# Kernel tuning notes

Measured on AMD Instinct MI355X. Metric: run time of the kernel, lower is better.

Reference implementation:

```python
import jax, jax.numpy as jnp
import numpy as np

N, E, G = 50000, 800000, 128          # nodes, edges, graphs
L, T, F = 4, 4, 20                    # conv layers, towers, per-tower width
D = T * F                             # 80 = hidden dim
EDGE_DIM = 16
AVG_DEG_LOG = float(np.log(17.0))     # avg_deg['log'] for avg in-degree ~16
EPS_STD = 1e-5
EPS_BN = 1e-5


def setup_inputs() -> dict:
    ks = iter(jax.random.split(jax.random.key(0), 32))
    rn = lambda *s: jax.random.normal(next(ks), s, jnp.float32) * 0.1
    return dict(
        x=jax.random.randint(next(ks), (N, 9), 0, 16),
        edge_index=jax.random.randint(next(ks), (2, E), 0, N),
        batch=jnp.sort(jax.random.randint(next(ks), (N,), 0, G)),
        edge_attr=rn(E, EDGE_DIM),
        atom_emb=rn(9, 16, D),
        edge_w=rn(L, EDGE_DIM, F), edge_b=jnp.zeros((L, F), jnp.float32),
        pre_w1=rn(L, T, 3 * F, F), pre_b1=jnp.zeros((L, T, F), jnp.float32),
        pre_w2=rn(L, T, F, F), pre_b2=jnp.zeros((L, T, F), jnp.float32),
        post_w1=rn(L, T, 13 * F, F), post_b1=jnp.zeros((L, T, F), jnp.float32),
        post_w2=rn(L, T, F, F), post_b2=jnp.zeros((L, T, F), jnp.float32),
        lin_w=rn(L, D, D), lin_b=jnp.zeros((L, D), jnp.float32),
        bn_g=jnp.ones((L, D), jnp.float32), bn_b=jnp.zeros((L, D), jnp.float32),
        mlp_w1=rn(D, 40), mlp_b1=jnp.zeros(40, jnp.float32),
        mlp_w2=rn(40, 20), mlp_b2=jnp.zeros(20, jnp.float32),
        mlp_w3=rn(20, 1), mlp_b3=jnp.zeros(1, jnp.float32),
    )


def _net(x, edge_index, batch, edge_attr, atom_emb, edge_w, edge_b, pre_w1,
         pre_b1, pre_w2, pre_b2, post_w1, post_b1, post_w2, post_b2, lin_w,
         lin_b, bn_g, bn_b, mlp_w1, mlp_b1, mlp_w2, mlp_b2, mlp_w3, mlp_b3):
    src, dst = edge_index[0], edge_index[1]
    # AtomEncoder: sum of 9 categorical embeddings -> [N, D]
    h = atom_emb[jnp.arange(9)[None, :], x].sum(1)
    deg_raw = jax.ops.segment_sum(jnp.ones((E,), jnp.float32), dst, N)
    deg = jnp.clip(deg_raw, 1.0)
    has_edge = (deg_raw > 0)[:, None, None]
    d3 = deg[:, None, None]
    logd = jnp.log(deg + 1.0)[:, None, None]
    for l in range(L):  # 4 PNAConv + BN + ReLU + residual (dropout off / eval)
        xt = h.reshape(N, T, F)
        ea = edge_attr @ edge_w[l] + edge_b[l]                      # [E, F]
        # message: concat(x_i, x_j, edge) -> per-tower pre MLP
        m = jnp.concatenate([xt[dst], xt[src],
                             jnp.broadcast_to(ea[:, None, :], (E, T, F))], -1)
        m = jax.nn.relu(jnp.einsum('eti,tio->eto', m, pre_w1[l]) + pre_b1[l])
        m = jnp.einsum('eti,tio->eto', m, pre_w2[l]) + pre_b2[l]    # [E,T,F]
        # multi-aggregator scatter-reduce
        mean = jax.ops.segment_sum(m, dst, N) / d3
        msq = jax.ops.segment_sum(m * m, dst, N) / d3
        std = jnp.sqrt(jax.nn.relu(msq - mean * mean) + EPS_STD)
        mn = jnp.where(has_edge, jax.ops.segment_min(m, dst, N), 0.0)
        mx = jnp.where(has_edge, jax.ops.segment_max(m, dst, N), 0.0)
        agg = jnp.concatenate([mean, mn, mx, std], -1)              # [N,T,4F]
        # degree scalers: identity, amplification, attenuation
        out = jnp.concatenate([agg, agg * (logd / AVG_DEG_LOG),
                               agg * (AVG_DEG_LOG / logd)], -1)     # [N,T,12F]
        out = jnp.concatenate([xt, out], -1)                        # [N,T,13F]
        out = jax.nn.relu(jnp.einsum('nti,tio->nto', out, post_w1[l]) + post_b1[l])
        out = jnp.einsum('nti,tio->nto', out, post_w2[l]) + post_b2[l]
        out = out.reshape(N, D) @ lin_w[l] + lin_b[l]
        # BatchNorm over nodes (batch statistics)
        mu = out.mean(0)
        var = jnp.mean((out - mu) ** 2, axis=0)
        out = (out - mu) * (bn_g[l] / jnp.sqrt(var + EPS_BN)) + bn_b[l]
        h = jax.nn.relu(out) + h
    # global mean pool over graphs + readout MLP
    cnt = jnp.clip(jax.ops.segment_sum(jnp.ones((N,), jnp.float32), batch, G), 1.0)
    g = jax.ops.segment_sum(h, batch, G) / cnt[:, None]
    g = jax.nn.relu(g @ mlp_w1 + mlp_b1)
    g = jax.nn.relu(g @ mlp_w2 + mlp_b2)
    return g @ mlp_w3 + mlp_b3                                      # [G, 1]


def reference(x, edge_index, batch, edge_attr, atom_emb, edge_w, edge_b, pre_w1,
              pre_b1, pre_w2, pre_b2, post_w1, post_b1, post_w2, post_b2, lin_w,
              lin_b, bn_g, bn_b, mlp_w1, mlp_b1, mlp_w2, mlp_b2, mlp_w3, mlp_b3):
    return _net(x, edge_index, batch, edge_attr, atom_emb, edge_w, edge_b, pre_w1,
                pre_b1, pre_w2, pre_b2, post_w1, post_b1, post_w2, post_b2,
                lin_w, lin_b, bn_g, bn_b, mlp_w1, mlp_b1, mlp_w2, mlp_b2,
                mlp_w3, mlp_b3)
```

## Files before the change

### kernel.cpp

```cpp
#include <hip/hip_runtime.h>
#include <hip/hip_bf16.h>

#define NN 50000
#define EE 800000
#define GG 128
#define LL 4
#define TT 4
#define FF 20
#define DD 80
#define SCAN_B ((NN + 1023) / 1024)
static constexpr float AVG_LOG = 2.8332133440562162f;

typedef __fp16 half2v __attribute__((ext_vector_type(2)));

__device__ __forceinline__ float bf2f(unsigned short u) {
  return __uint_as_float((unsigned)u << 16);
}
__device__ __forceinline__ unsigned short f2bf(float f) {
  __hip_bfloat16 b = __float2bfloat16(f);
  return *(unsigned short*)&b;
}
__device__ __forceinline__ half2v pkrtz(float a, float b) {
#if __has_builtin(__builtin_amdgcn_cvt_pkrtz)
  return __builtin_amdgcn_cvt_pkrtz(a, b);
#else
  half2v h; h.x = (__fp16)a; h.y = (__fp16)b; return h;
#endif
}
__device__ __forceinline__ float fdot2(half2v a, half2v b, float c) {
#if __has_builtin(__builtin_amdgcn_fdot2)
  return __builtin_amdgcn_fdot2(a, b, c, false);
#else
  return fmaf((float)a.x, (float)b.x, fmaf((float)a.y, (float)b.y, c));
#endif
}
__device__ __forceinline__ half2v u2h2(unsigned int u) {
  return __builtin_bit_cast(half2v, u);
}
__device__ __forceinline__ unsigned int h22u(half2v h) {
  return __builtin_bit_cast(unsigned int, h);
}
__device__ __forceinline__ unsigned int packh2_rne(float a, float b) {
  half2v h; h.x = (__fp16)a; h.y = (__fp16)b;
  return h22u(h);
}
__device__ __forceinline__ unsigned int pack_bf16(float a, float b) {
  return (unsigned int)f2bf(a) | ((unsigned int)f2bf(b) << 16);
}

__global__ __launch_bounds__(256) void k_h(const int* __restrict__ x,
                                           const float* __restrict__ atom_emb,
                                           float* __restrict__ h) {
  int idx = blockIdx.x * 256 + threadIdx.x;
  if (idx >= NN * DD) return;
  int n = idx / DD, d = idx - n * DD;
  const int* xr = x + n * 9;
  float acc = 0.f;
#pragma unroll
  for (int i = 0; i < 9; ++i) {
    int v = xr[i];
    acc += atom_emb[(i * 16 + v) * DD + d];
  }
  h[idx] = acc;
}

__global__ __launch_bounds__(256) void k_deg(const int* __restrict__ ei, int* __restrict__ cnt) {
  int e = blockIdx.x * 256 + threadIdx.x;
  if (e >= EE) return;
  atomicAdd(&cnt[ei[EE + e]], 1);
}

__global__ __launch_bounds__(1024) void k_scan_sum(const int* __restrict__ cnt, int* __restrict__ bsum) {
  __shared__ int red[1024];
  int tid = threadIdx.x;
  int i = blockIdx.x * 1024 + tid;
  red[tid] = (i < NN) ? cnt[i] : 0;
  __syncthreads();
  for (int off = 512; off > 0; off >>= 1) {
    if (tid < off) red[tid] += red[tid + off];
    __syncthreads();
  }
  if (tid == 0) bsum[blockIdx.x] = red[0];
}

__global__ void k_scan_top(const int* __restrict__ bsum, int* __restrict__ boff,
                           int* __restrict__ row_ptr) {
  if (threadIdx.x == 0 && blockIdx.x == 0) {
    int acc = 0;
    for (int b = 0; b < SCAN_B; ++b) { boff[b] = acc; acc += bsum[b]; }
    row_ptr[NN] = acc;
  }
}

__global__ __launch_bounds__(1024) void k_scan_apply(const int* __restrict__ cnt,
                                                     const int* __restrict__ boff,
                                                     int* __restrict__ row_ptr,
                                                     int* __restrict__ cursor) {
  __shared__ int sm[1024];
  int tid = threadIdx.x;
  int i = blockIdx.x * 1024 + tid;
  int v = (i < NN) ? cnt[i] : 0;
  sm[tid] = v;
  __syncthreads();
  for (int off = 1; off < 1024; off <<= 1) {
    int t = (tid >= off) ? sm[tid - off] : 0;
    __syncthreads();
    sm[tid] += t;
    __syncthreads();
  }
  int excl = boff[blockIdx.x] + sm[tid] - v;
  if (i < NN) { row_ptr[i] = excl; cursor[i] = excl; }
}

__global__ __launch_bounds__(256) void k_csrfill(const int* __restrict__ ei,
                                                 int* __restrict__ cursor,
                                                 int2* __restrict__ csr2,
                                                 int* __restrict__ csr_dst) {
  int e = blockIdx.x * 256 + threadIdx.x;
  if (e >= EE) return;
  int dst = ei[EE + e];
  int slot = atomicAdd(&cursor[dst], 1);
  csr2[slot] = make_int2(ei[e], e);
  csr_dst[slot] = dst;
}

__global__ __launch_bounds__(256) void k_eagather(const int2* __restrict__ csr2,
                                                  const float* __restrict__ edge_attr,
                                                  unsigned int* __restrict__ ea16) {
  int sl = blockIdx.x * 256 + threadIdx.x;
  if (sl >= EE) return;
  int e = csr2[sl].y;
  const float4* ap = (const float4*)(edge_attr + (size_t)e * 16);
  uint4 o0, o1;
  float4 v0 = ap[0], v1 = ap[1], v2 = ap[2], v3 = ap[3];
  o0.x = packh2_rne(v0.x, v0.y); o0.y = packh2_rne(v0.z, v0.w);
  o0.z = packh2_rne(v1.x, v1.y); o0.w = packh2_rne(v1.z, v1.w);
  o1.x = packh2_rne(v2.x, v2.y); o1.y = packh2_rne(v2.z, v2.w);
  o1.z = packh2_rne(v3.x, v3.y); o1.w = packh2_rne(v3.z, v3.w);
  uint4* op = (uint4*)(ea16 + (size_t)sl * 8);
  op[0] = o0; op[1] = o1;
}

__global__ __launch_bounds__(256) void k_nodeparams(const int* __restrict__ cnt,
                                                    float* __restrict__ inv_deg,
                                                    float* __restrict__ s1a,
                                                    float* __restrict__ s2a) {
  int n = blockIdx.x * 256 + threadIdx.x;
  if (n >= NN) return;
  int c = cnt[n];
  float deg = (c > 0) ? (float)c : 1.0f;
  inv_deg[n] = 1.0f / deg;
  float logd = logf(deg + 1.0f);
  s1a[n] = logd / AVG_LOG;
  s2a[n] = AVG_LOG / logd;
}

__global__ __launch_bounds__(64) void k_wcomb(const float* __restrict__ edge_w,
                                              const float* __restrict__ edge_b,
                                              const float* __restrict__ pre_w1,
                                              const float* __restrict__ pre_b1,
                                              const float* __restrict__ pre_w2,
                                              unsigned int* __restrict__ wcpk,
                                              unsigned int* __restrict__ w2pk,
                                              float* __restrict__ biasc, int l) {
  int t = blockIdx.x;
  int wt = l * TT + t;
  const float* W1 = pre_w1 + (size_t)wt * 1200;
  const float* W2 = pre_w2 + (size_t)wt * 400;
  const float* ew = edge_w + (size_t)l * 16 * FF;
  const float* eb = edge_b + (size_t)l * FF;
  int j = threadIdx.x;
  if (j >= FF) return;
  float col[16];
  for (int i = 0; i < 16; ++i) {
    float acc = 0.f;
#pragma unroll
    for (int f = 0; f < FF; ++f) acc = fmaf(ew[i * FF + f], W1[(40 + f) * FF + j], acc);
    col[i] = acc;
  }
#pragma unroll
  for (int i2 = 0; i2 < 8; ++i2)
    wcpk[((size_t)t * FF + j) * 8 + i2] = packh2_rne(col[2 * i2], col[2 * i2 + 1]);
#pragma unroll
  for (int i2 = 0; i2 < 10; ++i2)
    w2pk[((size_t)t * FF + j) * 10 + i2] = packh2_rne(W2[(2 * i2) * FF + j], W2[(2 * i2 + 1) * FF + j]);
  float b = pre_b1[wt * FF + j];
#pragma unroll
  for (int f = 0; f < FF; ++f) b = fmaf(eb[f], W1[(40 + f) * FF + j], b);
  biasc[t * FF + j] = b;
}

__global__ __launch_bounds__(64) void k_postpk(const float* __restrict__ post_w1,
                                               const float* __restrict__ post_w2,
                                               unsigned int* __restrict__ q1pk,
                                               unsigned int* __restrict__ q2pk, int l) {
  int t = blockIdx.x;
  int wt = l * TT + t;
  const float* Q1 = post_w1 + (size_t)wt * 5200;
  const float* Q2 = post_w2 + (size_t)wt * 400;
  int j = threadIdx.x;
  if (j >= FF) return;
  for (int i2 = 0; i2 < 120; ++i2) {
    int blk = i2 / 40, k = i2 - blk * 40;
    int r0 = 20 + 80 * blk + 2 * k;
    q1pk[((size_t)t * 120 + i2) * FF + j] = packh2_rne(Q1[r0 * FF + j], Q1[(r0 + 1) * FF + j]);
  }
#pragma unroll
  for (int i2 = 0; i2 < 10; ++i2)
    q2pk[((size_t)t * 10 + i2) * FF + j] = packh2_rne(Q2[(2 * i2) * FF + j], Q2[(2 * i2 + 1) * FF + j]);
}

__global__ __launch_bounds__(256) void k_prenode(
    const float* __restrict__ h, const float* __restrict__ pre_w1,
    const float* __restrict__ biasc,
    unsigned short* __restrict__ predD, unsigned short* __restrict__ predS, int l) {
  int tid = threadIdx.x;
  int t = tid >> 6, lane = tid & 63;
  int n = blockIdx.x * 64 + lane;
  if (n >= NN) return;
  int wt_u = __builtin_amdgcn_readfirstlane(l * TT + t);
  const float* W1 = pre_w1 + (size_t)wt_u * 1200;
  const float* bc = biasc + t * FF;
  float xt[FF];
  {
    const float4* pp = (const float4*)(h + (size_t)n * DD + t * FF);
#pragma unroll
    for (int i = 0; i < 5; ++i) { float4 v = pp[i]; xt[i*4]=v.x; xt[i*4+1]=v.y; xt[i*4+2]=v.z; xt[i*4+3]=v.w; }
  }
  float d[FF], s[FF];
#pragma unroll
  for (int j = 0; j < FF; ++j) { d[j] = bc[j]; s[j] = 0.f; }
#pragma unroll
  for (int i = 0; i < FF; ++i) {
    float a = xt[i];
#pragma unroll
    for (int j = 0; j < FF; ++j) {
      d[j] = fmaf(a, W1[i * FF + j], d[j]);
      s[j] = fmaf(a, W1[(FF + i) * FF + j], s[j]);
    }
  }
  ushort4* pd = (ushort4*)(predD + (size_t)n * DD + t * FF);
  ushort4* ps = (ushort4*)(predS + (size_t)n * DD + t * FF);
#pragma unroll
  for (int i = 0; i < 5; ++i) {
    pd[i] = make_ushort4(f2bf(d[i*4]), f2bf(d[i*4+1]), f2bf(d[i*4+2]), f2bf(d[i*4+3]));
    ps[i] = make_ushort4(f2bf(s[i*4]), f2bf(s[i*4+1]), f2bf(s[i*4+2]), f2bf(s[i*4+3]));
  }
}

__global__ __launch_bounds__(256, 4) void k_pre(
    const unsigned short* __restrict__ predD, const unsigned short* __restrict__ predS,
    const unsigned int* __restrict__ ea16,
    const int2* __restrict__ csr2, const int* __restrict__ csr_dst,
    const int* __restrict__ row_ptr,
    const unsigned int* __restrict__ wcpk,
    const unsigned int* __restrict__ w2pk,
    const float* __restrict__ pre_b2,
    unsigned int* __restrict__ m, int l, int n0, int n1, int capSlots) {
  int tid = threadIdx.x;
  int t = tid >> 6;
  int lane = tid & 63;
  int wt_u = __builtin_amdgcn_readfirstlane(l * TT + t);
  int t_u  = __builtin_amdgcn_readfirstlane(t);
  const unsigned int* Wcp = wcpk + (size_t)t_u * FF * 8;
  const unsigned int* W2p = w2pk + (size_t)t_u * FF * 10;
  const float* b2 = pre_b2 + (size_t)wt_u * FF;

  int sl = blockIdx.x * 64 + lane;
  int base = row_ptr[n0], end = row_ptr[n1];
  if (sl >= capSlots || base + sl >= end) return;
  int p = base + sl;
  int src = csr2[p].x;
  int dst = csr_dst[p];

  float m1[FF];
  {
    const ushort4* pp = (const ushort4*)(predD + (size_t)dst * DD + t * FF);
    const ushort4* qq = (const ushort4*)(predS + (size_t)src * DD + t * FF);
#pragma unroll
    for (int i = 0; i < 5; ++i) {
      ushort4 u = pp[i];
      ushort4 v = qq[i];
      m1[i*4+0] = bf2f(u.x) + bf2f(v.x);
      m1[i*4+1] = bf2f(u.y) + bf2f(v.y);
      m1[i*4+2] = bf2f(u.z) + bf2f(v.z);
      m1[i*4+3] = bf2f(u.w) + bf2f(v.w);
    }
  }
  half2v eap[8];
  {
    const uint4* ep = (const uint4*)(ea16 + (size_t)p * 8);
    uint4 e0 = ep[0], e1 = ep[1];
    eap[0] = u2h2(e0.x); eap[1] = u2h2(e0.y); eap[2] = u2h2(e0.z); eap[3] = u2h2(e0.w);
    eap[4] = u2h2(e1.x); eap[5] = u2h2(e1.y); eap[6] = u2h2(e1.z); eap[7] = u2h2(e1.w);
  }
#pragma unroll
  for (int j = 0; j < FF; ++j) {
    float c = m1[j];
#pragma unroll
    for (int i2 = 0; i2 < 8; ++i2) c = fdot2(eap[i2], u2h2(Wcp[j * 8 + i2]), c);
    m1[j] = c;
  }
  half2v mp[10];
#pragma unroll
  for (int pr = 0; pr < 10; ++pr)
    mp[pr] = pkrtz(fmaxf(m1[2*pr], 0.f), fmaxf(m1[2*pr+1], 0.f));
  float m2[FF];
#pragma unroll
  for (int j = 0; j < FF; ++j) {
    float c = b2[j];
#pragma unroll
    for (int i2 = 0; i2 < 10; ++i2) c = fdot2(mp[i2], u2h2(W2p[j * 10 + i2]), c);
    m2[j] = c;
  }
  unsigned int* mrow = m + (size_t)t * 10 * capSlots + sl;
#pragma unroll
  for (int pr = 0; pr < 10; ++pr)
    mrow[(size_t)pr * capSlots] = h22u(pkrtz(m2[2*pr], m2[2*pr+1]));
}

__global__ __launch_bounds__(320) void k_agg(
    const unsigned int* __restrict__ m,
    const int* __restrict__ row_ptr,
    const float* __restrict__ inv_deg,
    unsigned short* __restrict__ aggbuf, int n0, int n1, int capSlots) {
  int tid = threadIdx.x;
  int t = blockIdx.x & 3, tile = blockIdx.x >> 2;
  int ni = tid / 10, pr = tid - ni * 10;
  int n = n0 + tile * 32 + ni;
  if (n >= n1) return;
  int base = row_ptr[n0];
  int beg = row_ptr[n], end = row_ptr[n + 1];
  float inv = inv_deg[n];
  int s0 = beg - base, s1c = end - base;
  if (s0 < 0) s0 = 0;
  if (s1c > capSlots) s1c = capSlots;
  float sum0 = 0.f, sum1 = 0.f, sq0 = 0.f, sq1 = 0.f;
  float mn0 = 3.4e38f, mn1 = 3.4e38f, mx0 = -3.4e38f, mx1 = -3.4e38f;
  const unsigned int* mrow = m + (size_t)(t * 10 + pr) * capSlots;
  int p = s0;
  for (; p < s1c && (p & 3); ++p) {
    half2v h = u2h2(mrow[p]);
    float v0 = (float)h.x, v1 = (float)h.y;
    sum0 += v0; sq0 = fmaf(v0, v0, sq0); mn0 = fminf(mn0, v0); mx0 = fmaxf(mx0, v0);
    sum1 += v1; sq1 = fmaf(v1, v1, sq1); mn1 = fminf(mn1, v1); mx1 = fmaxf(mx1, v1);
  }
  for (; p + 4 <= s1c; p += 4) {
    uint4 q = *(const uint4*)(mrow + p);
#pragma unroll
    for (int k = 0; k < 4; ++k) {
      unsigned int u = (k == 0) ? q.x : (k == 1) ? q.y : (k == 2) ? q.z : q.w;
      half2v h = u2h2(u);
      float v0 = (float)h.x, v1 = (float)h.y;
      sum0 += v0; sq0 = fmaf(v0, v0, sq0); mn0 = fminf(mn0, v0); mx0 = fmaxf(mx0, v0);
      sum1 += v1; sq1 = fmaf(v1, v1, sq1); mn1 = fminf(mn1, v1); mx1 = fmaxf(mx1, v1);
    }
  }
  for (; p < s1c; ++p) {
    half2v h = u2h2(mrow[p]);
    float v0 = (float)h.x, v1 = (float)h.y;
    sum0 += v0; sq0 = fmaf(v0, v0, sq0); mn0 = fminf(mn0, v0); mx0 = fmaxf(mx0, v0);
    sum1 += v1; sq1 = fmaf(v1, v1, sq1); mn1 = fminf(mn1, v1); mx1 = fmaxf(mx1, v1);
  }
  float mu0 = sum0 * inv, mu1 = sum1 * inv;
  float sd0 = sqrtf(fmaxf(sq0 * inv - mu0 * mu0, 0.f) + 1e-5f);
  float sd1 = sqrtf(fmaxf(sq1 * inv - mu1 * mu1, 0.f) + 1e-5f);
  if (end <= beg) { mn0 = 0.f; mn1 = 0.f; mx0 = 0.f; mx1 = 0.f; }
  unsigned short* ab = aggbuf + ((size_t)(n - n0) * 4 + t) * 80;
  ((unsigned int*)(ab))[pr]      = pack_bf16(mu0, mu1);
  ((unsigned int*)(ab + 20))[pr] = pack_bf16(mn0, mn1);
  ((unsigned int*)(ab + 40))[pr] = pack_bf16(mx0, mx1);
  ((unsigned int*)(ab + 60))[pr] = pack_bf16(sd0, sd1);
}

__global__ __launch_bounds__(256) void k_post2(
    const float* __restrict__ h, const unsigned short* __restrict__ aggbuf,
    const float* __restrict__ s1a, const float* __restrict__ s2a,
    const float* __restrict__ post_w1, const float* __restrict__ post_b1,
    const unsigned int* __restrict__ q1pk, const unsigned int* __restrict__ q2pk,
    const float* __restrict__ post_b2,
    float* __restrict__ out2, int l, int n0, int n1, int tiles) {
  int t = blockIdx.x / tiles;
  int tile = blockIdx.x - t * tiles;
  int wt_u = l * TT + t;
  const float* Q1 = post_w1 + (size_t)wt_u * 5200;
  const float* B1 = post_b1 + (size_t)wt_u * FF;
  const float* B2 = post_b2 + (size_t)wt_u * FF;
  const unsigned int* q1 = q1pk + (size_t)t * 120 * FF;
  const unsigned int* q2 = q2pk + (size_t)t * 10 * FF;
  int n = n0 + tile * 256 + threadIdx.x;
  if (n >= n1) return;
  float c1 = s1a[n], c2 = s2a[n];
  half2v c1p = pkrtz(c1, c1), c2p = pkrtz(c2, c2);
  float xt[FF];
  {
    const float4* pp = (const float4*)(h + (size_t)n * DD + t * FF);
#pragma unroll
    for (int i = 0; i < 5; ++i) { float4 v = pp[i]; xt[i*4]=v.x; xt[i*4+1]=v.y; xt[i*4+2]=v.z; xt[i*4+3]=v.w; }
  }
  half2v a0p[40];
  {
    const uint4* ap = (const uint4*)(aggbuf + ((size_t)(n - n0) * 4 + t) * 80);
#pragma unroll
    for (int q = 0; q < 10; ++q) {
      uint4 v = ap[q];
      unsigned int w[4] = {v.x, v.y, v.z, v.w};
#pragma unroll
      for (int k = 0; k < 4; ++k) {
        unsigned int u = w[k];
        float lo = __uint_as_float(u << 16);
        float hi = __uint_as_float(u & 0xffff0000u);
        a0p[q * 4 + k] = pkrtz(lo, hi);
      }
    }
  }
  float o1[FF];
#pragma unroll
  for (int j = 0; j < FF; ++j) o1[j] = B1[j];
#pragma unroll
  for (int i = 0; i < FF; ++i) {
    float a = xt[i];
#pragma unroll
    for (int j = 0; j < FF; ++j) o1[j] = fmaf(a, Q1[i * FF + j], o1[j]);
  }
#pragma unroll 2
  for (int k = 0; k < 40; ++k) {
    half2v act = a0p[k];
    const unsigned int* wr = q1 + k * FF;
#pragma unroll
    for (int j = 0; j < FF; ++j) o1[j] = fdot2(act, u2h2(wr[j]), o1[j]);
  }
#pragma unroll 2
  for (int k = 0; k < 40; ++k) {
    half2v act = a0p[k] * c1p;
    const unsigned int* wr = q1 + (40 + k) * FF;
#pragma unroll
    for (int j = 0; j < FF; ++j) o1[j] = fdot2(act, u2h2(wr[j]), o1[j]);
  }
#pragma unroll 2
  for (int k = 0; k < 40; ++k) {
    half2v act = a0p[k] * c2p;
    const unsigned int* wr = q1 + (80 + k) * FF;
#pragma unroll
    for (int j = 0; j < FF; ++j) o1[j] = fdot2(act, u2h2(wr[j]), o1[j]);
  }
  half2v o1p[10];
#pragma unroll
  for (int i2 = 0; i2 < 10; ++i2)
    o1p[i2] = pkrtz(fmaxf(o1[2*i2], 0.f), fmaxf(o1[2*i2+1], 0.f));
  float o2[FF];
#pragma unroll
  for (int j = 0; j < FF; ++j) o2[j] = B2[j];
#pragma unroll 2
  for (int i2 = 0; i2 < 10; ++i2) {
    half2v act = o1p[i2];
    const unsigned int* wr = q2 + i2 * FF;
#pragma unroll
    for (int j = 0; j < FF; ++j) o2[j] = fdot2(act, u2h2(wr[j]), o2[j]);
  }
  float4* op = (float4*)(out2 + (size_t)n * DD + t * FF);
#pragma unroll
  for (int i = 0; i < 5; ++i) op[i] = make_float4(o2[i*4], o2[i*4+1], o2[i*4+2], o2[i*4+3]);
}

__global__ __launch_bounds__(320) void k_lin(const float* __restrict__ out2,
                                             const float* __restrict__ lin_w,
                                             const float* __restrict__ lin_b,
                                             float* __restrict__ outl,
                                             float* __restrict__ colsum, int l) {
  __shared__ float Wl[DD * DD];
  __shared__ float rowbuf[4 * DD];
  __shared__ float red[320];
  int tid = threadIdx.x;
  for (int i = tid; i < DD * DD; i += 320) Wl[i] = lin_w[(size_t)l * DD * DD + i];
  __syncthreads();
  int nl = tid / DD, d = tid - nl * DD;
  float bias = lin_b[l * DD + d];
  float bsum = 0.f, bsq = 0.f;
  for (int base = blockIdx.x * 4; base < NN; base += gridDim.x * 4) {
    int gi = base * DD + tid;
    rowbuf[tid] = (gi < NN * DD) ? out2[gi] : 0.f;
    __syncthreads();
    int n = base + nl;
    if (n < NN) {
      float acc = bias;
#pragma unroll
      for (int i = 0; i < DD; ++i) acc = fmaf(rowbuf[nl * DD + i], Wl[i * DD + d], acc);
      outl[(size_t)n * DD + d] = acc;
      bsum += acc; bsq += acc * acc;
    }
    __syncthreads();
  }
  red[tid] = bsum;
  __syncthreads();
  if (tid < DD) {
    float s = red[tid] + red[tid + DD] + red[tid + 2 * DD] + red[tid + 3 * DD];
    atomicAdd(&colsum[d], s);
  }
  __syncthreads();
  red[tid] = bsq;
  __syncthreads();
  if (tid < DD) {
    float s = red[tid] + red[tid + DD] + red[tid + 2 * DD] + red[tid + 3 * DD];
    atomicAdd(&colsum[DD + d], s);
  }
}

__global__ __launch_bounds__(128) void k_bnfinal(const float* __restrict__ colsum,
                                                 const float* __restrict__ bn_g,
                                                 const float* __restrict__ bn_b,
                                                 float* __restrict__ bnsc, int l) {
  int d = threadIdx.x;
  if (d >= DD) return;
  float mu = colsum[d] * (1.0f / NN);
  float var = colsum[DD + d] * (1.0f / NN) - mu * mu;
  float sc = bn_g[l * DD + d] * rsqrtf(var + 1e-5f);
  bnsc[d] = sc;
  bnsc[DD + d] = bn_b[l * DD + d] - mu * sc;
}

__global__ __launch_bounds__(256) void k_bnapply(const float* __restrict__ outl,
                                                 const float* __restrict__ bnsc,
                                                 float* __restrict__ h) {
  int idx = blockIdx.x * 256 + threadIdx.x;
  if (idx >= NN * DD) return;
  int d = idx % DD;
  float v = fmaf(outl[idx], bnsc[d], bnsc[DD + d]);
  h[idx] += fmaxf(v, 0.f);
}

__global__ __launch_bounds__(256) void k_gcnt(const int* __restrict__ batch, int* __restrict__ gcnt) {
  __shared__ int hcnt[GG];
  int tid = threadIdx.x;
  if (tid < GG) hcnt[tid] = 0;
  __syncthreads();
  int n = blockIdx.x * 256 + tid;
  if (n < NN) atomicAdd(&hcnt[batch[n]], 1);
  __syncthreads();
  if (tid < GG && hcnt[tid] > 0) atomicAdd(&gcnt[tid], hcnt[tid]);
}

__global__ void k_gstart(const int* __restrict__ gcnt, int* __restrict__ gstart) {
  if (threadIdx.x == 0 && blockIdx.x == 0) {
    int acc = 0;
    for (int g = 0; g < GG; ++g) { gstart[g] = acc; acc += gcnt[g]; }
  }
}

__global__ __launch_bounds__(320) void k_gmean(const float* __restrict__ h,
                                               const int* __restrict__ gstart,
                                               const int* __restrict__ gcnt,
                                               float* __restrict__ gbuf) {
  __shared__ float red[320];
  int g = blockIdx.x, tid = threadIdx.x;
  int nl = tid / DD, d = tid - nl * DD;
  int start = gstart[g], c = gcnt[g];
  float acc = 0.f;
  for (int r = start + nl; r < start + c; r += 4) acc += h[(size_t)r * DD + d];
  red[tid] = acc;
  __syncthreads();
  if (tid < DD) {
    float s = red[tid] + red[tid + DD] + red[tid + 2 * DD] + red[tid + 3 * DD];
    float cf = (c > 0) ? (float)c : 1.0f;
    gbuf[g * DD + tid] = s / cf;
  }
}

__global__ __launch_bounds__(64) void k_mlp(const float* __restrict__ gbuf,
                                            const float* __restrict__ w1, const float* __restrict__ b1,
                                            const float* __restrict__ w2, const float* __restrict__ b2,
                                            const float* __restrict__ w3, const float* __restrict__ b3,
                                            float* __restrict__ out) {
  __shared__ float row[DD];
  __shared__ float t1[40];
  __shared__ float t2[20];
  int g = blockIdx.x, tid = threadIdx.x;
  for (int i = tid; i < DD; i += 64) row[i] = gbuf[g * DD + i];
  __syncthreads();
  if (tid < 40) {
    float acc = b1[tid];
#pragma unroll
    for (int i = 0; i < DD; ++i) acc = fmaf(row[i], w1[i * 40 + tid], acc);
    t1[tid] = fmaxf(acc, 0.f);
  }
  __syncthreads();
  if (tid < 20) {
    float acc = b2[tid];
#pragma unroll
    for (int i = 0; i < 40; ++i) acc = fmaf(t1[i], w2[i * 20 + tid], acc);
    t2[tid] = fmaxf(acc, 0.f);
  }
  __syncthreads();
  if (tid == 0) {
    float acc = b3[0];
#pragma unroll
    for (int i = 0; i < 20; ++i) acc = fmaf(t2[i], w3[i], acc);
    out[g] = acc;
  }
}

extern "C" void kernel_launch(void* const* d_in, const int* in_sizes, int n_in,
                              void* d_out, int out_size, void* d_ws, size_t ws_size,
                              hipStream_t stream) {
  const int*   x         = (const int*)d_in[0];
  const int*   ei        = (const int*)d_in[1];
  const int*   batch     = (const int*)d_in[2];
  const float* edge_attr = (const float*)d_in[3];
  const float* atom_emb  = (const float*)d_in[4];
  const float* edge_w    = (const float*)d_in[5];
  const float* edge_b    = (const float*)d_in[6];
  const float* pre_w1    = (const float*)d_in[7];
  const float* pre_b1    = (const float*)d_in[8];
  const float* pre_w2    = (const float*)d_in[9];
  const float* pre_b2    = (const float*)d_in[10];
  const float* post_w1   = (const float*)d_in[11];
  const float* post_b1   = (const float*)d_in[12];
  const float* post_w2   = (const float*)d_in[13];
  const float* post_b2   = (const float*)d_in[14];
  const float* lin_w     = (const float*)d_in[15];
  const float* lin_b     = (const float*)d_in[16];
  const float* bn_g      = (const float*)d_in[17];
  const float* bn_b      = (const float*)d_in[18];
  const float* mlp_w1    = (const float*)d_in[19];
  const float* mlp_b1    = (const float*)d_in[20];
  const float* mlp_w2    = (const float*)d_in[21];
  const float* mlp_b2    = (const float*)d_in[22];
  const float* mlp_w3    = (const float*)d_in[23];
  const float* mlp_b3    = (const float*)d_in[24];
  float* out = (float*)d_out;

  char* ws = (char*)d_ws;
  size_t off = 0;
  auto alloc = [&](size_t bytes) -> void* {
    void* p = ws + off;
    off += (bytes + 15) & ~(size_t)15;
    return p;
  };
  float* h       = (float*)alloc((size_t)NN * DD * 4);
  float* out2    = (float*)alloc((size_t)NN * DD * 4);
  unsigned short* predD = (unsigned short*)alloc((size_t)NN * DD * 2);
  unsigned short* predS = (unsigned short*)alloc((size_t)NN * DD * 2);
  int2*  csr2    = (int2*)alloc((size_t)EE * 8);
  int*   csr_dst = (int*)alloc((size_t)EE * 4);
  unsigned int* ea16 = (unsigned int*)alloc((size_t)EE * 8 * 4);
  int*   row_ptr = (int*)alloc((size_t)(NN + 1) * 4);
  int*   cnt     = (int*)alloc((size_t)NN * 4);
  int*   cursor  = (int*)alloc((size_t)NN * 4);
  float* inv_deg = (float*)alloc((size_t)NN * 4);
  float* s1a     = (float*)alloc((size_t)NN * 4);
  float* s2a     = (float*)alloc((size_t)NN * 4);
  float* colsum  = (float*)alloc(2 * DD * 4);
  float* bnsc    = (float*)alloc(2 * DD * 4);
  float* gbuf    = (float*)alloc((size_t)GG * DD * 4);
  unsigned int* wcpk  = (unsigned int*)alloc((size_t)TT * FF * 8 * 4);
  unsigned int* w2pk  = (unsigned int*)alloc((size_t)TT * FF * 10 * 4);
  unsigned int* q1pk  = (unsigned int*)alloc((size_t)TT * 120 * FF * 4);
  unsigned int* q2pk  = (unsigned int*)alloc((size_t)TT * 10 * FF * 4);
  float* biasc   = (float*)alloc((size_t)TT * FF * 4);
  int*   bsum    = (int*)alloc((size_t)SCAN_B * 4);
  int*   boff    = (int*)alloc((size_t)SCAN_B * 4);
  int*   gcnt    = (int*)alloc((size_t)GG * 4);
  int*   gstart  = (int*)alloc((size_t)(GG + 1) * 4);
  (void)in_sizes; (void)n_in; (void)out_size;

  size_t rest = (ws_size > off) ? (ws_size - off) : 0;
  static const int cands[] = {1, 2, 4, 5, 8, 10, 20, 25, 40, 50};
  int c = -1, capSlots = 0, nodesPer = 0;
  size_t aggBytes = 0;
  for (int ci = 0; ci < 10; ++ci) {
    int cc = cands[ci];
    int np = (NN + cc - 1) / cc;
    size_t ab = ((size_t)np * 4 * 80 * 2 + 63) & ~(size_t)63;
    int slots = EE / cc + 25000; if (slots > EE) slots = EE;
    slots = (slots + 63) & ~63;
    size_t mb = (size_t)slots * DD * 2;
    if (ab + mb <= rest && ab + mb >= (size_t)NN * DD * 4) {
      c = cc; capSlots = slots; nodesPer = np; aggBytes = ab;
      break;
    }
  }
  if (c < 0) {
    c = 50; nodesPer = (NN + c - 1) / c;
    aggBytes = ((size_t)nodesPer * 4 * 80 * 2 + 63) & ~(size_t)63;
    size_t mb = (rest > aggBytes) ? rest - aggBytes : 0;
    capSlots = (int)(mb / (DD * 2)) & ~63;
  }
  unsigned short* aggbuf = (unsigned short*)(ws + off);
  unsigned int* mbuf = (unsigned int*)(ws + off + aggBytes);
  float* outl = (float*)(ws + off);

  hipMemsetAsync(cnt, 0, (size_t)NN * 4, stream);
  k_h<<<(NN * DD + 255) / 256, 256, 0, stream>>>(x, atom_emb, h);
  k_deg<<<(EE + 255) / 256, 256, 0, stream>>>(ei, cnt);
  k_scan_sum<<<SCAN_B, 1024, 0, stream>>>(cnt, bsum);
  k_scan_top<<<1, 64, 0, stream>>>(bsum, boff, row_ptr);
  k_scan_apply<<<SCAN_B, 1024, 0, stream>>>(cnt, boff, row_ptr, cursor);
  k_csrfill<<<(EE + 255) / 256, 256, 0, stream>>>(ei, cursor, csr2, csr_dst);
  k_eagather<<<(EE + 255) / 256, 256, 0, stream>>>(csr2, edge_attr, ea16);
  k_nodeparams<<<(NN + 255) / 256, 256, 0, stream>>>(cnt, inv_deg, s1a, s2a);

  for (int l = 0; l < LL; ++l) {
    k_wcomb<<<TT, 64, 0, stream>>>(edge_w, edge_b, pre_w1, pre_b1, pre_w2, wcpk, w2pk, biasc, l);
    k_postpk<<<TT, 64, 0, stream>>>(post_w1, post_w2, q1pk, q2pk, l);
    k_prenode<<<(NN + 63) / 64, 256, 0, stream>>>(h, pre_w1, biasc, predD, predS, l);
    for (int ck = 0; ck < c; ++ck) {
      int n0 = ck * nodesPer;
      int n1 = n0 + nodesPer; if (n1 > NN) n1 = NN;
      if (n0 >= n1) continue;
      int preBlocks = (capSlots + 63) / 64;
      k_pre<<<preBlocks, 256, 0, stream>>>(predD, predS, ea16, csr2, csr_dst, row_ptr,
          wcpk, w2pk, pre_b2, mbuf, l, n0, n1, capSlots);
      int aggBlocks = ((n1 - n0 + 31) / 32) * 4;
      k_agg<<<aggBlocks, 320, 0, stream>>>(mbuf, row_ptr, inv_deg, aggbuf, n0, n1, capSlots);
      int tiles = (n1 - n0 + 255) / 256;
      k_post2<<<tiles * TT, 256, 0, stream>>>(h, aggbuf, s1a, s2a,
          post_w1, post_b1, q1pk, q2pk, post_b2, out2, l, n0, n1, tiles);
    }
    hipMemsetAsync(colsum, 0, 2 * DD * 4, stream);
    k_lin<<<512, 320, 0, stream>>>(out2, lin_w, lin_b, outl, colsum, l);
    k_bnfinal<<<1, 128, 0, stream>>>(colsum, bn_g, bn_b, bnsc, l);
    k_bnapply<<<(NN * DD + 255) / 256, 256, 0, stream>>>(outl, bnsc, h);
  }

  hipMemsetAsync(gcnt, 0, (size_t)GG * 4, stream);
  k_gcnt<<<(NN + 255) / 256, 256, 0, stream>>>(batch, gcnt);
  k_gstart<<<1, 64, 0, stream>>>(gcnt, gstart);
  k_gmean<<<GG, 320, 0, stream>>>(h, gstart, gcnt, gbuf);
  k_mlp<<<GG, 64, 0, stream>>>(gbuf, mlp_w1, mlp_b1, mlp_w2, mlp_b2, mlp_w3, mlp_b3, out);
}
```

Baseline: 1.492 ms.

## Fuse per-edge message MLP with per-node aggregation via shared-memory tiles

Merges k_pre and k_agg into one k_preagg kernel. Each block handles a tile of 32 destination nodes for one tower, computes edge messages into shared memory, and reduces mean/min/max/std from there, so the per-edge message buffer no longer round-trips through global memory. The node-chunking loop over workspace capacity is removed and the aggregation buffer is allocated at full size. The CSR src/eid arrays are also split apart. The cost is lower parallelism per block, with 256-thread windows and barriers per window, and load imbalance across tiles whose degrees vary.

```diff
diff --git a/kernel.cpp b/kernel.cpp
--- a/kernel.cpp
+++ b/kernel.cpp
@@ -9,6 +9,7 @@
 #define FF 20
 #define DD 80
 #define SCAN_B ((NN + 1023) / 1024)
+#define TILE_N 32
 static constexpr float AVG_LOG = 2.8332133440562162f;
 
 typedef __fp16 half2v __attribute__((ext_vector_type(2)));
@@ -114,22 +115,24 @@
 
 __global__ __launch_bounds__(256) void k_csrfill(const int* __restrict__ ei,
                                                  int* __restrict__ cursor,
-                                                 int2* __restrict__ csr2,
+                                                 int* __restrict__ csr_src,
+                                                 int* __restrict__ csr_eid,
                                                  int* __restrict__ csr_dst) {
   int e = blockIdx.x * 256 + threadIdx.x;
   if (e >= EE) return;
   int dst = ei[EE + e];
   int slot = atomicAdd(&cursor[dst], 1);
-  csr2[slot] = make_int2(ei[e], e);
+  csr_src[slot] = ei[e];
+  csr_eid[slot] = e;
   csr_dst[slot] = dst;
 }
 
-__global__ __launch_bounds__(256) void k_eagather(const int2* __restrict__ csr2,
+__global__ __launch_bounds__(256) void k_eagather(const int* __restrict__ csr_eid,
                                                   const float* __restrict__ edge_attr,
                                                   unsigned int* __restrict__ ea16) {
   int sl = blockIdx.x * 256 + threadIdx.x;
   if (sl >= EE) return;
-  int e = csr2[sl].y;
+  int e = csr_eid[sl];
   const float4* ap = (const float4*)(edge_attr + (size_t)e * 16);
   uint4 o0, o1;
   float4 v0 = ap[0], v1 = ap[1], v2 = ap[2], v3 = ap[3];
@@ -248,129 +251,157 @@
   }
 }
 
-__global__ __launch_bounds__(256, 4) void k_pre(
-    const unsigned short* __restrict__ predD, const unsigned short* __restrict__ predS,
+__global__ __launch_bounds__(256) void k_preagg(
+    const unsigned short* __restrict__ predD,
+    const unsigned short* __restrict__ predS,
     const unsigned int* __restrict__ ea16,
-    const int2* __restrict__ csr2, const int* __restrict__ csr_dst,
+    const int* __restrict__ csr_src,
+    const int* __restrict__ csr_dst,
     const int* __restrict__ row_ptr,
+    const float* __restrict__ inv_deg,
     const unsigned int* __restrict__ wcpk,
     const unsigned int* __restrict__ w2pk,
     const float* __restrict__ pre_b2,
-    unsigned int* __restrict__ m, int l, int n0, int n1, int capSlots) {
+    unsigned short* __restrict__ aggbuf,
+    int l, int tiles) {
+  __shared__ int nbr[TILE_N + 1];
+  __shared__ float dDs[TILE_N * FF];
+  __shared__ unsigned int m2w[256 * 11];
   int tid = threadIdx.x;
-  int t = tid >> 6;
-  int lane = tid & 63;
-  int wt_u = __builtin_amdgcn_readfirstlane(l * TT + t);
-  int t_u  = __builtin_amdgcn_readfirstlane(t);
-  const unsigned int* Wcp = wcpk + (size_t)t_u * FF * 8;
-  const unsigned int* W2p = w2pk + (size_t)t_u * FF * 10;
-  const float* b2 = pre_b2 + (size_t)wt_u * FF;
-
-  int sl = blockIdx.x * 64 + lane;
-  int base = row_ptr[n0], end = row_ptr[n1];
-  if (sl >= capSlots || base + sl >= end) return;
-  int p = base + sl;
-  int src = csr2[p].x;
-  int dst = csr_dst[p];
-
-  float m1[FF];
+  int t = blockIdx.x / tiles;
+  int tile = blockIdx.x - t * tiles;
+  int n0 = tile * TILE_N;
+  const unsigned int* Wcp = wcpk + (size_t)t * FF * 8;
+  const unsigned int* W2p = w2pk + (size_t)t * FF * 10;
+  const float* b2 = pre_b2 + (size_t)(l * TT + t) * FF;
+
+  if (tid <= TILE_N) {
+    int node = n0 + tid; if (node > NN) node = NN;
+    nbr[tid] = row_ptr[node];
+  }
+  for (int i = tid; i < TILE_N * FF; i += 256) {
+    int ni = i / FF, ch = i - ni * FF;
+    int node = n0 + ni;
+    dDs[i] = (node < NN) ? bf2f(predD[(size_t)node * DD + t * FF + ch]) : 0.f;
+  }
+  __syncthreads();
+  int tbeg = nbr[0], tend = nbr[TILE_N];
+
+  int ni0 = tid / 10, pr0 = tid - ni0 * 10;
+  int it1 = 256 + tid;
+  int ni1 = it1 / 10, pr1 = it1 - ni1 * 10;
+  bool has1 = (tid < TILE_N * 10 - 256);
+  int begA = nbr[ni0], endA = nbr[ni0 + 1];
+  int begB = has1 ? nbr[ni1] : 0, endB = has1 ? nbr[ni1 + 1] : 0;
+  float a_s0=0.f,a_s1=0.f,a_q0=0.f,a_q1=0.f,a_n0=3.4e38f,a_n1=3.4e38f,a_x0=-3.4e38f,a_x1=-3.4e38f;
+  float b_s0=0.f,b_s1=0.f,b_q0=0.f,b_q1=0.f,b_n0=3.4e38f,b_n1=3.4e38f,b_x0=-3.4e38f,b_x1=-3.4e38f;
+
+  for (int wb = tbeg; wb < tend; wb += 256) {
+    int p = wb + tid;
+    if (p < tend) {
+      int src = csr_src[p];
+      int ni = csr_dst[p] - n0;
+      float m1[FF];
+      {
+        const float4* dd = (const float4*)(dDs + ni * FF);
+        const ushort4* qq = (const ushort4*)(predS + (size_t)src * DD + t * FF);
+#pragma unroll
+        for (int i = 0; i < 5; ++i) {
+          float4 d4 = dd[i];
+          ushort4 v = qq[i];
+          m1[i*4+0] = d4.x + bf2f(v.x);
+          m1[i*4+1] = d4.y + bf2f(v.y);
+          m1[i*4+2] = d4.z + bf2f(v.z);
+          m1[i*4+3] = d4.w + bf2f(v.w);
+        }
+      }
+      half2v eap[8];
+      {
+        const uint4* ep = (const uint4*)(ea16 + (size_t)p * 8);
+        uint4 e0 = ep[0], e1 = ep[1];
+        eap[0] = u2h2(e0.x); eap[1] = u2h2(e0.y); eap[2] = u2h2(e0.z); eap[3] = u2h2(e0.w);
+        eap[4] = u2h2(e1.x); eap[5] = u2h2(e1.y); eap[6] = u2h2(e1.z); eap[7] = u2h2(e1.w);
+      }
+#pragma unroll
+      for (int j = 0; j < FF; ++j) {
+        float c = m1[j];
+#pragma unroll
+        for (int i2 = 0; i2 < 8; ++i2) c = fdot2(eap[i2], u2h2(Wcp[j * 8 + i2]), c);
+        m1[j] = c;
+      }
+      half2v mp[10];
+#pragma unroll
+      for (int pr = 0; pr < 10; ++pr)
+        mp[pr] = pkrtz(fmaxf(m1[2*pr], 0.f), fmaxf(m1[2*pr+1], 0.f));
+      float m2[FF];
+#pragma unroll
+      for (int j = 0; j < FF; ++j) {
+        float c = b2[j];
+#pragma unroll
+        for (int i2 = 0; i2 < 10; ++i2) c = fdot2(mp[i2], u2h2(W2p[j * 10 + i2]), c);
+        m2[j] = c;
+      }
+      unsigned int* row = m2w + tid * 11;
+#pragma unroll
+      for (int pr = 0; pr < 10; ++pr) row[pr] = h22u(pkrtz(m2[2*pr], m2[2*pr+1]));
+    }
+    __syncthreads();
+    int we = (wb + 256 < tend) ? (wb + 256) : tend;
+    {
+      int lo = begA > wb ? begA : wb;
+      int hi = endA < we ? endA : we;
+      for (int s = lo; s < hi; ++s) {
+        half2v h2 = u2h2(m2w[(s - wb) * 11 + pr0]);
+        float v0 = (float)h2.x, v1 = (float)h2.y;
+        a_s0 += v0; a_q0 = fmaf(v0, v0, a_q0); a_n0 = fminf(a_n0, v0); a_x0 = fmaxf(a_x0, v0);
+        a_s1 += v1; a_q1 = fmaf(v1, v1, a_q1); a_n1 = fminf(a_n1, v1); a_x1 = fmaxf(a_x1, v1);
+      }
+    }
+    if (has1) {
+      int lo = begB > wb ? begB : wb;
+      int hi = endB < we ? endB : we;
+      for (int s = lo; s < hi; ++s) {
+        half2v h2 = u2h2(m2w[(s - wb) * 11 + pr1]);
+        float v0 = (float)h2.x, v1 = (float)h2.y;
+        b_s0 += v0; b_q0 = fmaf(v0, v0, b_q0); b_n0 = fminf(b_n0, v0); b_x0 = fmaxf(b_x0, v0);
+        b_s1 += v1; b_q1 = fmaf(v1, v1, b_q1); b_n1 = fminf(b_n1, v1); b_x1 = fmaxf(b_x1, v1);
+      }
+    }
+    __syncthreads();
+  }
+
   {
-    const ushort4* pp = (const ushort4*)(predD + (size_t)dst * DD + t * FF);
-    const ushort4* qq = (const ushort4*)(predS + (size_t)src * DD + t * FF);
-#pragma unroll
-    for (int i = 0; i < 5; ++i) {
-      ushort4 u = pp[i];
-      ushort4 v = qq[i];
-      m1[i*4+0] = bf2f(u.x) + bf2f(v.x);
-      m1[i*4+1] = bf2f(u.y) + bf2f(v.y);
-      m1[i*4+2] = bf2f(u.z) + bf2f(v.z);
-      m1[i*4+3] = bf2f(u.w) + bf2f(v.w);
+    int n = n0 + ni0;
+    if (n < NN) {
+      float inv = inv_deg[n];
+      float mu0 = a_s0 * inv, mu1 = a_s1 * inv;
+      float sd0 = sqrtf(fmaxf(a_q0 * inv - mu0 * mu0, 0.f) + 1e-5f);
+      float sd1 = sqrtf(fmaxf(a_q1 * inv - mu1 * mu1, 0.f) + 1e-5f);
+      float mn0 = a_n0, mn1 = a_n1, mx0 = a_x0, mx1 = a_x1;
+      if (endA <= begA) { mn0 = 0.f; mn1 = 0.f; mx0 = 0.f; mx1 = 0.f; }
+      unsigned short* ab = aggbuf + ((size_t)n * 4 + t) * 80;
+      ((unsigned int*)(ab))[pr0]      = pack_bf16(mu0, mu1);
+      ((unsigned int*)(ab + 20))[pr0] = pack_bf16(mn0, mn1);
+      ((unsigned int*)(ab + 40))[pr0] = pack_bf16(mx0, mx1);
+      ((unsigned int*)(ab + 60))[pr0] = pack_bf16(sd0, sd1);
     }
   }
-  half2v eap[8];
-  {
-    const uint4* ep = (const uint4*)(ea16 + (size_t)p * 8);
-    uint4 e0 = ep[0], e1 = ep[1];
-    eap[0] = u2h2(e0.x); eap[1] = u2h2(e0.y); eap[2] = u2h2(e0.z); eap[3] = u2h2(e0.w);
-    eap[4] = u2h2(e1.x); eap[5] = u2h2(e1.y); eap[6] = u2h2(e1.z); eap[7] = u2h2(e1.w);
-  }
-#pragma unroll
-  for (int j = 0; j < FF; ++j) {
-    float c = m1[j];
-#pragma unroll
-    for (int i2 = 0; i2 < 8; ++i2) c = fdot2(eap[i2], u2h2(Wcp[j * 8 + i2]), c);
-    m1[j] = c;
-  }
-  half2v mp[10];
-#pragma unroll
-  for (int pr = 0; pr < 10; ++pr)
-    mp[pr] = pkrtz(fmaxf(m1[2*pr], 0.f), fmaxf(m1[2*pr+1], 0.f));
-  float m2[FF];
-#pragma unroll
-  for (int j = 0; j < FF; ++j) {
-    float c = b2[j];
-#pragma unroll
-    for (int i2 = 0; i2 < 10; ++i2) c = fdot2(mp[i2], u2h2(W2p[j * 10 + i2]), c);
-    m2[j] = c;
-  }
-  unsigned int* mrow = m + (size_t)t * 10 * capSlots + sl;
-#pragma unroll
-  for (int pr = 0; pr < 10; ++pr)
-    mrow[(size_t)pr * capSlots] = h22u(pkrtz(m2[2*pr], m2[2*pr+1]));
-}
-
-__global__ __launch_bounds__(320) void k_agg(
-    const unsigned int* __restrict__ m,
-    const int* __restrict__ row_ptr,
-    const float* __restrict__ inv_deg,
-    unsigned short* __restrict__ aggbuf, int n0, int n1, int capSlots) {
-  int tid = threadIdx.x;
-  int t = blockIdx.x & 3, tile = blockIdx.x >> 2;
-  int ni = tid / 10, pr = tid - ni * 10;
-  int n = n0 + tile * 32 + ni;
-  if (n >= n1) return;
-  int base = row_ptr[n0];
-  int beg = row_ptr[n], end = row_ptr[n + 1];
-  float inv = inv_deg[n];
-  int s0 = beg - base, s1c = end - base;
-  if (s0 < 0) s0 = 0;
-  if (s1c > capSlots) s1c = capSlots;
-  float sum0 = 0.f, sum1 = 0.f, sq0 = 0.f, sq1 = 0.f;
-  float mn0 = 3.4e38f, mn1 = 3.4e38f, mx0 = -3.4e38f, mx1 = -3.4e38f;
-  const unsigned int* mrow = m + (size_t)(t * 10 + pr) * capSlots;
-  int p = s0;
-  for (; p < s1c && (p & 3); ++p) {
-    half2v h = u2h2(mrow[p]);
-    float v0 = (float)h.x, v1 = (float)h.y;
-    sum0 += v0; sq0 = fmaf(v0, v0, sq0); mn0 = fminf(mn0, v0); mx0 = fmaxf(mx0, v0);
-    sum1 += v1; sq1 = fmaf(v1, v1, sq1); mn1 = fminf(mn1, v1); mx1 = fmaxf(mx1, v1);
-  }
-  for (; p + 4 <= s1c; p += 4) {
-    uint4 q = *(const uint4*)(mrow + p);
-#pragma unroll
-    for (int k = 0; k < 4; ++k) {
-      unsigned int u = (k == 0) ? q.x : (k == 1) ? q.y : (k == 2) ? q.z : q.w;
-      half2v h = u2h2(u);
-      float v0 = (float)h.x, v1 = (float)h.y;
-      sum0 += v0; sq0 = fmaf(v0, v0, sq0); mn0 = fminf(mn0, v0); mx0 = fmaxf(mx0, v0);
-      sum1 += v1; sq1 = fmaf(v1, v1, sq1); mn1 = fminf(mn1, v1); mx1 = fmaxf(mx1, v1);
+  if (has1) {
+    int n = n0 + ni1;
+    if (n < NN) {
+      float inv = inv_deg[n];
+      float mu0 = b_s0 * inv, mu1 = b_s1 * inv;
+      float sd0 = sqrtf(fmaxf(b_q0 * inv - mu0 * mu0, 0.f) + 1e-5f);
+      float sd1 = sqrtf(fmaxf(b_q1 * inv - mu1 * mu1, 0.f) + 1e-5f);
+      float mn0 = b_n0, mn1 = b_n1, mx0 = b_x0, mx1 = b_x1;
+      if (endB <= begB) { mn0 = 0.f; mn1 = 0.f; mx0 = 0.f; mx1 = 0.f; }
+      unsigned short* ab = aggbuf + ((size_t)n * 4 + t) * 80;
+      ((unsigned int*)(ab))[pr1]      = pack_bf16(mu0, mu1);
+      ((unsigned int*)(ab + 20))[pr1] = pack_bf16(mn0, mn1);
+      ((unsigned int*)(ab + 40))[pr1] = pack_bf16(mx0, mx1);
+      ((unsigned int*)(ab + 60))[pr1] = pack_bf16(sd0, sd1);
     }
   }
-  for (; p < s1c; ++p) {
-    half2v h = u2h2(mrow[p]);
-    float v0 = (float)h.x, v1 = (float)h.y;
-    sum0 += v0; sq0 = fmaf(v0, v0, sq0); mn0 = fminf(mn0, v0); mx0 = fmaxf(mx0, v0);
-    sum1 += v1; sq1 = fmaf(v1, v1, sq1); mn1 = fminf(mn1, v1); mx1 = fmaxf(mx1, v1);
-  }
-  float mu0 = sum0 * inv, mu1 = sum1 * inv;
-  float sd0 = sqrtf(fmaxf(sq0 * inv - mu0 * mu0, 0.f) + 1e-5f);
-  float sd1 = sqrtf(fmaxf(sq1 * inv - mu1 * mu1, 0.f) + 1e-5f);
-  if (end <= beg) { mn0 = 0.f; mn1 = 0.f; mx0 = 0.f; mx1 = 0.f; }
-  unsigned short* ab = aggbuf + ((size_t)(n - n0) * 4 + t) * 80;
-  ((unsigned int*)(ab))[pr]      = pack_bf16(mu0, mu1);
-  ((unsigned int*)(ab + 20))[pr] = pack_bf16(mn0, mn1);
-  ((unsigned int*)(ab + 40))[pr] = pack_bf16(mx0, mx1);
-  ((unsigned int*)(ab + 60))[pr] = pack_bf16(sd0, sd1);
 }
 
 __global__ __launch_bounds__(256) void k_post2(
@@ -379,7 +410,7 @@
     const float* __restrict__ post_w1, const float* __restrict__ post_b1,
     const unsigned int* __restrict__ q1pk, const unsigned int* __restrict__ q2pk,
     const float* __restrict__ post_b2,
-    float* __restrict__ out2, int l, int n0, int n1, int tiles) {
+    float* __restrict__ out2, int l, int tiles) {
   int t = blockIdx.x / tiles;
   int tile = blockIdx.x - t * tiles;
   int wt_u = l * TT + t;
@@ -388,8 +419,8 @@
   const float* B2 = post_b2 + (size_t)wt_u * FF;
   const unsigned int* q1 = q1pk + (size_t)t * 120 * FF;
   const unsigned int* q2 = q2pk + (size_t)t * 10 * FF;
-  int n = n0 + tile * 256 + threadIdx.x;
-  if (n >= n1) return;
+  int n = tile * 256 + threadIdx.x;
+  if (n >= NN) return;
   float c1 = s1a[n], c2 = s2a[n];
   half2v c1p = pkrtz(c1, c1), c2p = pkrtz(c2, c2);
   float xt[FF];
@@ -400,7 +431,7 @@
   }
   half2v a0p[40];
   {
-    const uint4* ap = (const uint4*)(aggbuf + ((size_t)(n - n0) * 4 + t) * 80);
+    const uint4* ap = (const uint4*)(aggbuf + ((size_t)n * 4 + t) * 80);
 #pragma unroll
     for (int q = 0; q < 10; ++q) {
       uint4 v = ap[q];
@@ -640,7 +671,8 @@
   float* out2    = (float*)alloc((size_t)NN * DD * 4);
   unsigned short* predD = (unsigned short*)alloc((size_t)NN * DD * 2);
   unsigned short* predS = (unsigned short*)alloc((size_t)NN * DD * 2);
-  int2*  csr2    = (int2*)alloc((size_t)EE * 8);
+  int*   csr_src = (int*)alloc((size_t)EE * 4);
+  int*   csr_eid = (int*)alloc((size_t)EE * 4);
   int*   csr_dst = (int*)alloc((size_t)EE * 4);
   unsigned int* ea16 = (unsigned int*)alloc((size_t)EE * 8 * 4);
   int*   row_ptr = (int*)alloc((size_t)(NN + 1) * 4);
@@ -661,33 +693,9 @@
   int*   boff    = (int*)alloc((size_t)SCAN_B * 4);
   int*   gcnt    = (int*)alloc((size_t)GG * 4);
   int*   gstart  = (int*)alloc((size_t)(GG + 1) * 4);
-  (void)in_sizes; (void)n_in; (void)out_size;
-
-  size_t rest = (ws_size > off) ? (ws_size - off) : 0;
-  static const int cands[] = {1, 2, 4, 5, 8, 10, 20, 25, 40, 50};
-  int c = -1, capSlots = 0, nodesPer = 0;
-  size_t aggBytes = 0;
-  for (int ci = 0; ci < 10; ++ci) {
-    int cc = cands[ci];
-    int np = (NN + cc - 1) / cc;
-    size_t ab = ((size_t)np * 4 * 80 * 2 + 63) & ~(size_t)63;
-    int slots = EE / cc + 25000; if (slots > EE) slots = EE;
-    slots = (slots + 63) & ~63;
-    size_t mb = (size_t)slots * DD * 2;
-    if (ab + mb <= rest && ab + mb >= (size_t)NN * DD * 4) {
-      c = cc; capSlots = slots; nodesPer = np; aggBytes = ab;
-      break;
-    }
-  }
-  if (c < 0) {
-    c = 50; nodesPer = (NN + c - 1) / c;
-    aggBytes = ((size_t)nodesPer * 4 * 80 * 2 + 63) & ~(size_t)63;
-    size_t mb = (rest > aggBytes) ? rest - aggBytes : 0;
-    capSlots = (int)(mb / (DD * 2)) & ~63;
-  }
-  unsigned short* aggbuf = (unsigned short*)(ws + off);
-  unsigned int* mbuf = (unsigned int*)(ws + off + aggBytes);
-  float* outl = (float*)(ws + off);
+  unsigned short* aggbuf = (unsigned short*)alloc((size_t)NN * 4 * 80 * 2);
+  float* outl = (float*)aggbuf;
+  (void)in_sizes; (void)n_in; (void)out_size; (void)ws_size;
 
   hipMemsetAsync(cnt, 0, (size_t)NN * 4, stream);
   k_h<<<(NN * DD + 255) / 256, 256, 0, stream>>>(x, atom_emb, h);
@@ -695,27 +703,20 @@
   k_scan_sum<<<SCAN_B, 1024, 0, stream>>>(cnt, bsum);
   k_scan_top<<<1, 64, 0, stream>>>(bsum, boff, row_ptr);
   k_scan_apply<<<SCAN_B, 1024, 0, stream>>>(cnt, boff, row_ptr, cursor);
-  k_csrfill<<<(EE + 255) / 256, 256, 0, stream>>>(ei, cursor, csr2, csr_dst);
-  k_eagather<<<(EE + 255) / 256, 256, 0, stream>>>(csr2, edge_attr, ea16);
+  k_csrfill<<<(EE + 255) / 256, 256, 0, stream>>>(ei, cursor, csr_src, csr_eid, csr_dst);
+  k_eagather<<<(EE + 255) / 256, 256, 0, stream>>>(csr_eid, edge_attr, ea16);
   k_nodeparams<<<(NN + 255) / 256, 256, 0, stream>>>(cnt, inv_deg, s1a, s2a);
 
+  int tilesA = (NN + TILE_N - 1) / TILE_N;
+  int tilesP = (NN + 255) / 256;
   for (int l = 0; l < LL; ++l) {
     k_wcomb<<<TT, 64, 0, stream>>>(edge_w, edge_b, pre_w1, pre_b1, pre_w2, wcpk, w2pk, biasc, l);
     k_postpk<<<TT, 64, 0, stream>>>(post_w1, post_w2, q1pk, q2pk, l);
     k_prenode<<<(NN + 63) / 64, 256, 0, stream>>>(h, pre_w1, biasc, predD, predS, l);
-    for (int ck = 0; ck < c; ++ck) {
-      int n0 = ck * nodesPer;
-      int n1 = n0 + nodesPer; if (n1 > NN) n1 = NN;
-      if (n0 >= n1) continue;
-      int preBlocks = (capSlots + 63) / 64;
-      k_pre<<<preBlocks, 256, 0, stream>>>(predD, predS, ea16, csr2, csr_dst, row_ptr,
-          wcpk, w2pk, pre_b2, mbuf, l, n0, n1, capSlots);
-      int aggBlocks = ((n1 - n0 + 31) / 32) * 4;
-      k_agg<<<aggBlocks, 320, 0, stream>>>(mbuf, row_ptr, inv_deg, aggbuf, n0, n1, capSlots);
-      int tiles = (n1 - n0 + 255) / 256;
-      k_post2<<<tiles * TT, 256, 0, stream>>>(h, aggbuf, s1a, s2a,
-          post_w1, post_b1, q1pk, q2pk, post_b2, out2, l, n0, n1, tiles);
-    }
+    k_preagg<<<tilesA * TT, 256, 0, stream>>>(predD, predS, ea16, csr_src, csr_dst, row_ptr,
+        inv_deg, wcpk, w2pk, pre_b2, aggbuf, l, tilesA);
+    k_post2<<<tilesP * TT, 256, 0, stream>>>(h, aggbuf, s1a, s2a,
+        post_w1, post_b1, q1pk, q2pk, post_b2, out2, l, tilesP);
     hipMemsetAsync(colsum, 0, 2 * DD * 4, stream);
     k_lin<<<512, 320, 0, stream>>>(out2, lin_w, lin_b, outl, colsum, l);
     k_bnfinal<<<1, 128, 0, stream>>>(colsum, bn_g, bn_b, bnsc, l);
```

New measurement: 1.452 ms. 2.7% less time.
